# Performance work log

Hardware: AMD Instinct MI355X
Metric: run time of the kernel (lower is better)

The kernel has to match this reference:

```python
import jax, jax.numpy as jnp
import numpy as np


def setup_inputs() -> dict:
    key = jax.random.key(0)
    k1, k2 = jax.random.split(key)
    B, HW, C = 256, 196, 384
    x = jax.random.normal(k1, (B, HW + 1, C), dtype=jnp.float32)
    edge_aggregation = jax.random.normal(k2, (B, HW, C), dtype=jnp.float32)
    return {"x": x, "edge_aggregation": edge_aggregation}


def reference(x, edge_aggregation):
    # x: (B, HW+1, C); edge_aggregation: (B, HW, C)
    nodes = x[:, 1:]                                    # (B, HW, C)
    # AvgPool1d over full HW length == mean over token axis
    ea = jnp.mean(edge_aggregation, axis=1, keepdims=True)   # (B, 1, C)
    channel_importance = jax.nn.sigmoid(ea)                  # (B, 1, C)
    # nodes @ channel_importance^T -> (B, HW, 1); keep as (B, HW)
    channel_aggregation = jnp.einsum('bnc,bc->bn', nodes, channel_importance[:, 0])
    # ascending sort indices per sample (matches torch.sort default)
    idx = jnp.argsort(channel_aggregation, axis=1)           # (B, HW)
    nodes_sorted = jnp.take_along_axis(nodes, idx[:, :, None], axis=1)  # (B, HW, C)
    HW = nodes.shape[1]
    start = HW // 4 * 3                                       # keep top quartile
    nodes_pooled = nodes_sorted[:, start:]                    # (B, HW - start, C)
    out = jnp.concatenate([x[:, :1], nodes_pooled], axis=1)   # (B, HW-start+1, C)
    return out
```

## Files before the change

### kernel.cpp

```cpp
#include <hip/hip_runtime.h>
#include <math.h>

#define NB      256
#define NNODES  196
#define NC      384
#define SEQ     197
#define START   147
#define KEEP    49
#define OUTROWS 50

#define NT      960
#define NWAVE   15
#define RG      10
#define C4      96

__global__ __launch_bounds__(NT)
void pooling_block_kernel(const float* __restrict__ x,
                          const float* __restrict__ ea,
                          float* __restrict__ out) {
    __shared__ double partial[RG][NC];
    __shared__ alignas(16) float imp[NC];
    __shared__ float scores[NNODES];
    __shared__ int   sel[KEEP];

    const int b   = blockIdx.x;
    const int tid = threadIdx.x;

    {
        const int rg = tid / C4;
        const int c4 = tid % C4;
        const float4* p = (const float4*)(ea + (size_t)b * NNODES * NC);
        double ax = 0.0, ay = 0.0, az = 0.0, aw = 0.0;
        for (int row = rg; row < NNODES; row += RG) {
            float4 v = p[(size_t)row * C4 + c4];
            ax += v.x; ay += v.y; az += v.z; aw += v.w;
        }
        partial[rg][4 * c4 + 0] = ax;
        partial[rg][4 * c4 + 1] = ay;
        partial[rg][4 * c4 + 2] = az;
        partial[rg][4 * c4 + 3] = aw;
    }
    __syncthreads();
    if (tid < NC) {
        double s = 0.0;
        #pragma unroll
        for (int rg = 0; rg < RG; ++rg) s += partial[rg][tid];
        float m = (float)(s * (1.0 / (double)NNODES));
        imp[tid] = 1.0f / (1.0f + expf(-m));
    }
    __syncthreads();

    const int wave = tid >> 6;
    const int lane = tid & 63;
    const float* nodes = x + ((size_t)b * SEQ + 1) * NC;

    for (int n = wave; n < NNODES; n += NWAVE) {
        const float2* row2 = (const float2*)(nodes + (size_t)n * NC);
        const float2* imp2 = (const float2*)imp;
        double acc = 0.0;
        #pragma unroll
        for (int j = 0; j < 3; ++j) {
            int i = lane + 64 * j;
            float2 v = row2[i];
            float2 w = imp2[i];
            acc += (double)v.x * (double)w.x + (double)v.y * (double)w.y;
        }
        #pragma unroll
        for (int off = 32; off > 0; off >>= 1)
            acc += __shfl_xor(acc, off);
        if (lane == 0) scores[n] = (float)acc;
    }
    __syncthreads();

    if (tid < NNODES) {
        const float s = scores[tid];
        int rank = 0;
        for (int m = 0; m < NNODES; ++m) {
            const float sm = scores[m];
            rank += (sm < s) || (sm == s && m < tid);
        }
        if (rank >= START) sel[rank - START] = tid;
    }
    __syncthreads();

    {
        const int jg = tid / C4;
        const int c4 = tid % C4;
        const float4* nodes4 = (const float4*)nodes;
        const float4* cls4   = (const float4*)(x + (size_t)b * SEQ * NC);
        float4* out4         = (float4*)(out + (size_t)b * OUTROWS * NC);
        #pragma unroll
        for (int it = 0; it < 5; ++it) {
            int j = jg + RG * it;
            const float4* src = (j == 0) ? cls4 : (nodes4 + (size_t)sel[j - 1] * C4);
            out4[(size_t)j * C4 + c4] = src[c4];
        }
    }
}

extern "C" void kernel_launch(void* const* d_in, const int* in_sizes, int n_in,
                              void* d_out, int out_size, void* d_ws, size_t ws_size,
                              hipStream_t stream) {
    const float* x   = (const float*)d_in[0];
    const float* ea  = (const float*)d_in[1];
    float* out       = (float*)d_out;

    hipLaunchKernelGGL(pooling_block_kernel,
                       dim3(NB), dim3(NT), 0, stream,
                       x, ea, out);
}
```

Before: 36.21 us.

## Split fused per-sample kernel into three kernels for wider parallelism

Replaces the single 256-block fused kernel with three launches: a column-sum kernel over 7 row chunks per sample, a score kernel over 6 node chunks per sample, and a rank-and-gather kernel. Partial sums and scores now go through workspace memory. The goal is to fill more CUs on the GPU, since 256 blocks underuse it. The cost is two extra kernel launches and the extra global round-trips for partials and scores. It also adds a float rounding of the partial sums.

```diff
diff --git a/kernel.cpp b/kernel.cpp
--- a/kernel.cpp
+++ b/kernel.cpp
@@ -8,43 +8,58 @@
 #define START   147
 #define KEEP    49
 #define OUTROWS 50
-
-#define NT      960
-#define NWAVE   15
-#define RG      10
 #define C4      96
 
-__global__ __launch_bounds__(NT)
-void pooling_block_kernel(const float* __restrict__ x,
-                          const float* __restrict__ ea,
-                          float* __restrict__ out) {
-    __shared__ double partial[RG][NC];
+#define NCH     7
+#define RPC     28
+
+#define QCH     6
+#define NPQ     33
+
+#define WS_PARTIALS_ELEMS  ((size_t)NB * NCH * NC)
+#define WS_SCORES_OFF      WS_PARTIALS_ELEMS
+
+__global__ __launch_bounds__(384)
+void k1_colsum(const float* __restrict__ ea, float* __restrict__ partials) {
+    __shared__ double acc[4][NC];
+    const int bid = blockIdx.x;
+    const int b   = bid / NCH;
+    const int k   = bid % NCH;
+    const int tid = threadIdx.x;
+    const int c4  = tid % C4;
+    const int rg  = tid / C4;
+
+    const float4* p = (const float4*)(ea + (size_t)b * NNODES * NC) + c4;
+    double ax = 0.0, ay = 0.0, az = 0.0, aw = 0.0;
+    #pragma unroll
+    for (int i = 0; i < 7; ++i) {
+        int row = k * RPC + rg + 4 * i;
+        float4 v = p[(size_t)row * C4];
+        ax += v.x; ay += v.y; az += v.z; aw += v.w;
+    }
+    acc[rg][4 * c4 + 0] = ax;
+    acc[rg][4 * c4 + 1] = ay;
+    acc[rg][4 * c4 + 2] = az;
+    acc[rg][4 * c4 + 3] = aw;
+    __syncthreads();
+    double s = acc[0][tid] + acc[1][tid] + acc[2][tid] + acc[3][tid];
+    partials[(size_t)bid * NC + tid] = (float)s;
+}
+
+__global__ __launch_bounds__(384)
+void k2_scores(const float* __restrict__ x, const float* __restrict__ partials,
+               float* __restrict__ scores) {
     __shared__ alignas(16) float imp[NC];
-    __shared__ float scores[NNODES];
-    __shared__ int   sel[KEEP];
-
-    const int b   = blockIdx.x;
+    const int bid = blockIdx.x;
+    const int b   = bid / QCH;
+    const int q   = bid % QCH;
     const int tid = threadIdx.x;
 
     {
-        const int rg = tid / C4;
-        const int c4 = tid % C4;
-        const float4* p = (const float4*)(ea + (size_t)b * NNODES * NC);
-        double ax = 0.0, ay = 0.0, az = 0.0, aw = 0.0;
-        for (int row = rg; row < NNODES; row += RG) {
-            float4 v = p[(size_t)row * C4 + c4];
-            ax += v.x; ay += v.y; az += v.z; aw += v.w;
-        }
-        partial[rg][4 * c4 + 0] = ax;
-        partial[rg][4 * c4 + 1] = ay;
-        partial[rg][4 * c4 + 2] = az;
-        partial[rg][4 * c4 + 3] = aw;
-    }
-    __syncthreads();
-    if (tid < NC) {
         double s = 0.0;
         #pragma unroll
-        for (int rg = 0; rg < RG; ++rg) s += partial[rg][tid];
+        for (int k = 0; k < NCH; ++k)
+            s += (double)partials[((size_t)b * NCH + k) * NC + tid];
         float m = (float)(s * (1.0 / (double)NNODES));
         imp[tid] = 1.0f / (1.0f + expf(-m));
     }
@@ -53,59 +68,74 @@
     const int wave = tid >> 6;
     const int lane = tid & 63;
     const float* nodes = x + ((size_t)b * SEQ + 1) * NC;
+    const float2* imp2 = (const float2*)imp;
 
-    for (int n = wave; n < NNODES; n += NWAVE) {
+    float2 w[3];
+    #pragma unroll
+    for (int j = 0; j < 3; ++j) w[j] = imp2[lane + 64 * j];
+
+    const int nend = (q * NPQ + NPQ < NNODES) ? q * NPQ + NPQ : NNODES;
+    for (int n = q * NPQ + wave; n < nend; n += 6) {
         const float2* row2 = (const float2*)(nodes + (size_t)n * NC);
-        const float2* imp2 = (const float2*)imp;
         double acc = 0.0;
         #pragma unroll
         for (int j = 0; j < 3; ++j) {
-            int i = lane + 64 * j;
-            float2 v = row2[i];
-            float2 w = imp2[i];
-            acc += (double)v.x * (double)w.x + (double)v.y * (double)w.y;
+            float2 v = row2[lane + 64 * j];
+            acc += (double)v.x * (double)w[j].x + (double)v.y * (double)w[j].y;
         }
         #pragma unroll
         for (int off = 32; off > 0; off >>= 1)
             acc += __shfl_xor(acc, off);
-        if (lane == 0) scores[n] = (float)acc;
+        if (lane == 0) scores[(size_t)b * NNODES + n] = (float)acc;
     }
+}
+
+__global__ __launch_bounds__(960)
+void k3_rank_gather(const float* __restrict__ x, const float* __restrict__ scores,
+                    float* __restrict__ out) {
+    __shared__ float sc[NNODES];
+    __shared__ int   sel[KEEP];
+    const int b   = blockIdx.x;
+    const int tid = threadIdx.x;
+
+    if (tid < NNODES) sc[tid] = scores[(size_t)b * NNODES + tid];
     __syncthreads();
 
     if (tid < NNODES) {
-        const float s = scores[tid];
+        const float s = sc[tid];
         int rank = 0;
         for (int m = 0; m < NNODES; ++m) {
-            const float sm = scores[m];
+            const float sm = sc[m];
             rank += (sm < s) || (sm == s && m < tid);
         }
         if (rank >= START) sel[rank - START] = tid;
     }
     __syncthreads();
 
-    {
-        const int jg = tid / C4;
-        const int c4 = tid % C4;
-        const float4* nodes4 = (const float4*)nodes;
-        const float4* cls4   = (const float4*)(x + (size_t)b * SEQ * NC);
-        float4* out4         = (float4*)(out + (size_t)b * OUTROWS * NC);
-        #pragma unroll
-        for (int it = 0; it < 5; ++it) {
-            int j = jg + RG * it;
-            const float4* src = (j == 0) ? cls4 : (nodes4 + (size_t)sel[j - 1] * C4);
-            out4[(size_t)j * C4 + c4] = src[c4];
-        }
+    const int jg = tid / C4;
+    const int c4 = tid % C4;
+    const float* nodes   = x + ((size_t)b * SEQ + 1) * NC;
+    const float4* nodes4 = (const float4*)nodes;
+    const float4* cls4   = (const float4*)(x + (size_t)b * SEQ * NC);
+    float4* out4         = (float4*)(out + (size_t)b * OUTROWS * NC);
+    #pragma unroll
+    for (int it = 0; it < 5; ++it) {
+        int j = jg + 10 * it;
+        const float4* src = (j == 0) ? cls4 : (nodes4 + (size_t)sel[j - 1] * C4);
+        out4[(size_t)j * C4 + c4] = src[c4];
     }
 }
 
 extern "C" void kernel_launch(void* const* d_in, const int* in_sizes, int n_in,
                               void* d_out, int out_size, void* d_ws, size_t ws_size,
                               hipStream_t stream) {
-    const float* x   = (const float*)d_in[0];
-    const float* ea  = (const float*)d_in[1];
-    float* out       = (float*)d_out;
+    const float* x  = (const float*)d_in[0];
+    const float* ea = (const float*)d_in[1];
+    float* out      = (float*)d_out;
+    float* partials = (float*)d_ws;
+    float* scores   = (float*)d_ws + WS_SCORES_OFF;
 
-    hipLaunchKernelGGL(pooling_block_kernel,
-                       dim3(NB), dim3(NT), 0, stream,
-                       x, ea, out);
+    hipLaunchKernelGGL(k1_colsum,      dim3(NB * NCH), dim3(384), 0, stream, ea, partials);
+    hipLaunchKernelGGL(k2_scores,      dim3(NB * QCH), dim3(384), 0, stream, x, partials, scores);
+    hipLaunchKernelGGL(k3_rank_gather, dim3(NB),       dim3(960), 0, stream, x, scores, out);
 }
```

New measurement: 45.41 us. +25.4%, slower.

## Overlap node-row staging into LDS with edge-aggregation mean reduction

Applied to the files above, without the earlier changes.

The block is split so that 576 threads reduce the edge-aggregation mean while the other 384 threads copy the first 88 node rows into a shared-memory stage buffer at the same time. The scoring and gather phases then read those rows from LDS instead of global memory, and the remaining rows still come from global. The goal is to overlap the node loads with the reduction and avoid repeated global reads of the same rows. In exchange the kernel uses about 135KB of LDS per block, which limits occupancy to one block per CU. The reduction partials are also stored as float instead of double, a small precision change.

```diff
diff --git a/kernel.cpp b/kernel.cpp
--- a/kernel.cpp
+++ b/kernel.cpp
@@ -8,75 +8,98 @@
 #define START   147
 #define KEEP    49
 #define OUTROWS 50
+#define C4      96
 
 #define NT      960
-#define NWAVE   15
-#define RG      10
-#define C4      96
+#define P1T     576
+#define P1RG    6
+#define SROWS   88
+#define SITERS  22
 
 __global__ __launch_bounds__(NT)
-void pooling_block_kernel(const float* __restrict__ x,
-                          const float* __restrict__ ea,
-                          float* __restrict__ out) {
-    __shared__ double partial[RG][NC];
+void pool_fused(const float* __restrict__ x,
+                const float* __restrict__ ea,
+                float* __restrict__ out) {
+    __shared__ alignas(16) float stage[SROWS][NC];
+    __shared__ float partial[P1RG][NC];
     __shared__ alignas(16) float imp[NC];
-    __shared__ float scores[NNODES];
+    __shared__ float sc[NNODES];
     __shared__ int   sel[KEEP];
 
-    const int b   = blockIdx.x;
-    const int tid = threadIdx.x;
+    const int b    = blockIdx.x;
+    const int tid  = threadIdx.x;
+    const int wave = tid >> 6;
+    const int lane = tid & 63;
+    const float* nodes = x + ((size_t)b * SEQ + 1) * NC;
 
-    {
+    if (tid < P1T) {
         const int rg = tid / C4;
         const int c4 = tid % C4;
-        const float4* p = (const float4*)(ea + (size_t)b * NNODES * NC);
+        const float4* p = (const float4*)(ea + (size_t)b * NNODES * NC) + c4;
         double ax = 0.0, ay = 0.0, az = 0.0, aw = 0.0;
-        for (int row = rg; row < NNODES; row += RG) {
-            float4 v = p[(size_t)row * C4 + c4];
+        for (int row = rg; row < NNODES; row += P1RG) {
+            float4 v = p[(size_t)row * C4];
             ax += v.x; ay += v.y; az += v.z; aw += v.w;
         }
-        partial[rg][4 * c4 + 0] = ax;
-        partial[rg][4 * c4 + 1] = ay;
-        partial[rg][4 * c4 + 2] = az;
-        partial[rg][4 * c4 + 3] = aw;
+        partial[rg][4 * c4 + 0] = (float)ax;
+        partial[rg][4 * c4 + 1] = (float)ay;
+        partial[rg][4 * c4 + 2] = (float)az;
+        partial[rg][4 * c4 + 3] = (float)aw;
+    } else {
+        const int t = tid - P1T;
+        const float4* src = (const float4*)nodes;
+        float4* dst = (float4*)&stage[0][0];
+        #pragma unroll
+        for (int i = 0; i < SITERS; ++i)
+            dst[t + 384 * i] = src[t + 384 * i];
     }
     __syncthreads();
+
     if (tid < NC) {
         double s = 0.0;
         #pragma unroll
-        for (int rg = 0; rg < RG; ++rg) s += partial[rg][tid];
+        for (int rg = 0; rg < P1RG; ++rg) s += (double)partial[rg][tid];
         float m = (float)(s * (1.0 / (double)NNODES));
         imp[tid] = 1.0f / (1.0f + expf(-m));
     }
     __syncthreads();
 
-    const int wave = tid >> 6;
-    const int lane = tid & 63;
-    const float* nodes = x + ((size_t)b * SEQ + 1) * NC;
+    {
+        const float2* imp2 = (const float2*)imp;
+        float2 w[3];
+        #pragma unroll
+        for (int j = 0; j < 3; ++j) w[j] = imp2[lane + 64 * j];
 
-    for (int n = wave; n < NNODES; n += NWAVE) {
-        const float2* row2 = (const float2*)(nodes + (size_t)n * NC);
-        const float2* imp2 = (const float2*)imp;
-        double acc = 0.0;
-        #pragma unroll
-        for (int j = 0; j < 3; ++j) {
-            int i = lane + 64 * j;
-            float2 v = row2[i];
-            float2 w = imp2[i];
-            acc += (double)v.x * (double)w.x + (double)v.y * (double)w.y;
+        for (int n = wave; n < NNODES; n += 15) {
+            double acc = 0.0;
+            if (n < SROWS) {
+                const float2* row2 = (const float2*)&stage[n][0];
+                #pragma unroll
+                for (int j = 0; j < 3; ++j) {
+                    float2 v = row2[lane + 64 * j];
+                    acc += (double)v.x * (double)w[j].x + (double)v.y * (double)w[j].y;
+                }
+            } else {
+                const float2* row2 = (const float2*)(nodes + (size_t)n * NC);
+                #pragma unroll
+                for (int j = 0; j < 3; ++j) {
+                    float2 v = row2[lane + 64 * j];
+                    acc += (double)v.x * (double)w[j].x + (double)v.y * (double)w[j].y;
+                }
+            }
+            #pragma unroll
+            for (int off = 32; off > 0; off >>= 1)
+                acc += __shfl_xor(acc, off);
+            if (lane == 0) sc[n] = (float)acc;
         }
-        #pragma unroll
-        for (int off = 32; off > 0; off >>= 1)
-            acc += __shfl_xor(acc, off);
-        if (lane == 0) scores[n] = (float)acc;
     }
     __syncthreads();
 
     if (tid < NNODES) {
-        const float s = scores[tid];
+        const float s = sc[tid];
         int rank = 0;
         for (int m = 0; m < NNODES; ++m) {
-            const float sm = scores[m];
+            const float sm = sc[m];
             rank += (sm < s) || (sm == s && m < tid);
         }
         if (rank >= START) sel[rank - START] = tid;
@@ -91,9 +114,16 @@
         float4* out4         = (float4*)(out + (size_t)b * OUTROWS * NC);
         #pragma unroll
         for (int it = 0; it < 5; ++it) {
-            int j = jg + RG * it;
-            const float4* src = (j == 0) ? cls4 : (nodes4 + (size_t)sel[j - 1] * C4);
-            out4[(size_t)j * C4 + c4] = src[c4];
+            int j = jg + 10 * it;
+            float4 v;
+            if (j == 0) {
+                v = cls4[c4];
+            } else {
+                int n = sel[j - 1];
+                v = (n < SROWS) ? ((const float4*)&stage[n][0])[c4]
+                                : nodes4[(size_t)n * C4 + c4];
+            }
+            out4[(size_t)j * C4 + c4] = v;
         }
     }
 }
@@ -101,11 +131,9 @@
 extern "C" void kernel_launch(void* const* d_in, const int* in_sizes, int n_in,
                               void* d_out, int out_size, void* d_ws, size_t ws_size,
                               hipStream_t stream) {
-    const float* x   = (const float*)d_in[0];
-    const float* ea  = (const float*)d_in[1];
-    float* out       = (float*)d_out;
+    const float* x  = (const float*)d_in[0];
+    const float* ea = (const float*)d_in[1];
+    float* out      = (float*)d_out;
 
-    hipLaunchKernelGGL(pooling_block_kernel,
-                       dim3(NB), dim3(NT), 0, stream,
-                       x, ea, out);
+    hipLaunchKernelGGL(pool_fused, dim3(NB), dim3(NT), 0, stream, x, ea, out);
 }
```

Result: slower. 40.49 us (+11.8%).

## Split each sample across two blocks with atomic score merge and spin barrier

Applied to the files above, without the earlier changes.

Each batch sample is now handled by a pair of blocks. Each block reduces half of the channels for the mean and the dot-product scores, then merges its partial scores through global atomics and a per-sample flag spin-wait before ranking, and copies half of the output rows. This doubles the grid from 256 to 512 blocks so more of the GPU's compute units have work. In exchange it adds a workspace memset, global atomics, and an inter-block spin barrier that can deadlock if the two blocks of a pair are not co-resident. Summing the two partial scores in float can also change score rounding and therefore tie order.

```diff
diff --git a/kernel.cpp b/kernel.cpp
--- a/kernel.cpp
+++ b/kernel.cpp
@@ -8,31 +8,42 @@
 #define START   147
 #define KEEP    49
 #define OUTROWS 50
+#define C4      96
 
 #define NT      960
-#define NWAVE   15
-#define RG      10
-#define C4      96
+#define CH      192
+#define C4H     48
+#define RG1     20
+
+#define SCORE_BYTES ((size_t)NB * NNODES * sizeof(float))
+#define FLAG_BYTES  ((size_t)NB * sizeof(int))
 
 __global__ __launch_bounds__(NT)
-void pooling_block_kernel(const float* __restrict__ x,
-                          const float* __restrict__ ea,
-                          float* __restrict__ out) {
-    __shared__ double partial[RG][NC];
-    __shared__ alignas(16) float imp[NC];
-    __shared__ float scores[NNODES];
+void pool_pair(const float* __restrict__ x,
+               const float* __restrict__ ea,
+               float* __restrict__ out,
+               float* __restrict__ score,
+               int*   __restrict__ flag) {
+    __shared__ double partial[RG1][CH];
+    __shared__ float imp[CH];
+    __shared__ float psc[NNODES];
+    __shared__ float sc[NNODES];
     __shared__ int   sel[KEEP];
 
-    const int b   = blockIdx.x;
-    const int tid = threadIdx.x;
+    const int gb   = blockIdx.x;
+    const int b    = gb >> 1;
+    const int h    = gb & 1;
+    const int tid  = threadIdx.x;
+    const int wave = tid >> 6;
+    const int lane = tid & 63;
 
     {
-        const int rg = tid / C4;
-        const int c4 = tid % C4;
-        const float4* p = (const float4*)(ea + (size_t)b * NNODES * NC);
+        const int rg = tid / C4H;
+        const int c4 = tid % C4H;
+        const float4* p = (const float4*)(ea + (size_t)b * NNODES * NC) + h * C4H + c4;
         double ax = 0.0, ay = 0.0, az = 0.0, aw = 0.0;
-        for (int row = rg; row < NNODES; row += RG) {
-            float4 v = p[(size_t)row * C4 + c4];
+        for (int row = rg; row < NNODES; row += RG1) {
+            float4 v = p[(size_t)row * C4];
             ax += v.x; ay += v.y; az += v.z; aw += v.w;
         }
         partial[rg][4 * c4 + 0] = ax;
@@ -41,42 +52,53 @@
         partial[rg][4 * c4 + 3] = aw;
     }
     __syncthreads();
-    if (tid < NC) {
+    if (tid < CH) {
         double s = 0.0;
         #pragma unroll
-        for (int rg = 0; rg < RG; ++rg) s += partial[rg][tid];
+        for (int rg = 0; rg < RG1; ++rg) s += partial[rg][tid];
         float m = (float)(s * (1.0 / (double)NNODES));
         imp[tid] = 1.0f / (1.0f + expf(-m));
     }
     __syncthreads();
 
-    const int wave = tid >> 6;
-    const int lane = tid & 63;
-    const float* nodes = x + ((size_t)b * SEQ + 1) * NC;
-
-    for (int n = wave; n < NNODES; n += NWAVE) {
-        const float2* row2 = (const float2*)(nodes + (size_t)n * NC);
-        const float2* imp2 = (const float2*)imp;
-        double acc = 0.0;
-        #pragma unroll
-        for (int j = 0; j < 3; ++j) {
-            int i = lane + 64 * j;
-            float2 v = row2[i];
-            float2 w = imp2[i];
-            acc += (double)v.x * (double)w.x + (double)v.y * (double)w.y;
+    {
+        const float w0 = imp[lane];
+        const float w1 = imp[lane + 64];
+        const float w2 = imp[lane + 128];
+        const float* xb = x + ((size_t)b * SEQ + 1) * NC + h * CH;
+        for (int n = wave; n < NNODES; n += 15) {
+            const float* row = xb + (size_t)n * NC;
+            double acc = (double)row[lane]       * (double)w0
+                       + (double)row[lane + 64]  * (double)w1
+                       + (double)row[lane + 128] * (double)w2;
+            #pragma unroll
+            for (int off = 32; off > 0; off >>= 1)
+                acc += __shfl_xor(acc, off);
+            if (lane == 0) psc[n] = (float)acc;
         }
-        #pragma unroll
-        for (int off = 32; off > 0; off >>= 1)
-            acc += __shfl_xor(acc, off);
-        if (lane == 0) scores[n] = (float)acc;
     }
     __syncthreads();
 
+    if (tid < NNODES) atomicAdd(&score[(size_t)b * NNODES + tid], psc[tid]);
+    __syncthreads();
+    if (tid == 0) {
+        __threadfence();
+        __hip_atomic_fetch_add(&flag[b], 1, __ATOMIC_RELEASE, __HIP_MEMORY_SCOPE_AGENT);
+        long spins = 0;
+        while (__hip_atomic_load(&flag[b], __ATOMIC_ACQUIRE, __HIP_MEMORY_SCOPE_AGENT) < 2
+               && spins < (1L << 31)) ++spins;
+    }
+    __syncthreads();
+    if (tid < NNODES)
+        sc[tid] = __hip_atomic_load(&score[(size_t)b * NNODES + tid],
+                                    __ATOMIC_RELAXED, __HIP_MEMORY_SCOPE_AGENT);
+    __syncthreads();
+
     if (tid < NNODES) {
-        const float s = scores[tid];
+        const float s = sc[tid];
         int rank = 0;
         for (int m = 0; m < NNODES; ++m) {
-            const float sm = scores[m];
+            const float sm = sc[m];
             rank += (sm < s) || (sm == s && m < tid);
         }
         if (rank >= START) sel[rank - START] = tid;
@@ -86,14 +108,18 @@
     {
         const int jg = tid / C4;
         const int c4 = tid % C4;
+        const float* nodes   = x + ((size_t)b * SEQ + 1) * NC;
         const float4* nodes4 = (const float4*)nodes;
         const float4* cls4   = (const float4*)(x + (size_t)b * SEQ * NC);
         float4* out4         = (float4*)(out + (size_t)b * OUTROWS * NC);
         #pragma unroll
-        for (int it = 0; it < 5; ++it) {
-            int j = jg + RG * it;
-            const float4* src = (j == 0) ? cls4 : (nodes4 + (size_t)sel[j - 1] * C4);
-            out4[(size_t)j * C4 + c4] = src[c4];
+        for (int it = 0; it < 3; ++it) {
+            int jj = jg + 10 * it;
+            if (jj < 25) {
+                int j = h * 25 + jj;
+                const float4* src = (j == 0) ? cls4 : (nodes4 + (size_t)sel[j - 1] * C4);
+                out4[(size_t)j * C4 + c4] = src[c4];
+            }
         }
     }
 }
@@ -101,11 +127,14 @@
 extern "C" void kernel_launch(void* const* d_in, const int* in_sizes, int n_in,
                               void* d_out, int out_size, void* d_ws, size_t ws_size,
                               hipStream_t stream) {
-    const float* x   = (const float*)d_in[0];
-    const float* ea  = (const float*)d_in[1];
-    float* out       = (float*)d_out;
+    const float* x  = (const float*)d_in[0];
+    const float* ea = (const float*)d_in[1];
+    float* out      = (float*)d_out;
+    float* score    = (float*)d_ws;
+    int*   flag     = (int*)((char*)d_ws + SCORE_BYTES);
 
-    hipLaunchKernelGGL(pooling_block_kernel,
-                       dim3(NB), dim3(NT), 0, stream,
-                       x, ea, out);
+    hipMemsetAsync(d_ws, 0, SCORE_BYTES + FLAG_BYTES, stream);
+
+    hipLaunchKernelGGL(pool_pair, dim3(NB * 2), dim3(NT), 0, stream,
+                       x, ea, out, score, flag);
 }
```

Result: slower. 73.24 us (+102.3%).
